# Kernel tuning notes

Measured on AMD Instinct MI355X. Metric: run time of the kernel, lower is better.

Reference implementation:

```python
import jax, jax.numpy as jnp
import numpy as np

HIDDEN = 4096
N_HEADS = 32
N_KV_HEADS = 8
HEAD_DIM = HIDDEN // N_HEADS  # 128
GROUPS = N_HEADS // N_KV_HEADS  # 4
SEQ = 2048


def setup_inputs() -> dict:
    key = jax.random.key(0)
    k1, k2, k3 = jax.random.split(key, 3)
    positions = jnp.arange(SEQ, dtype=jnp.int32)
    hidden_states = jax.random.normal(k1, (SEQ, HIDDEN), dtype=jnp.float32) * 0.02
    Wqkv = jax.random.normal(k2, (HIDDEN, (N_HEADS + 2 * N_KV_HEADS) * HEAD_DIM), dtype=jnp.float32) * 0.02
    Wo = jax.random.normal(k3, (N_HEADS * HEAD_DIM, HIDDEN), dtype=jnp.float32) * 0.02
    return {"positions": positions, "hidden_states": hidden_states, "Wqkv": Wqkv, "Wo": Wo}


def reference(positions, hidden_states, Wqkv, Wo):
    # forward unsqueezes to batch=1: x [1, S, D]
    x = hidden_states[None]
    S = x.shape[1]
    scale = HEAD_DIM ** -0.5

    qkv = jnp.einsum('bsd,de->bse', x, Wqkv)  # [1, S, (H + 2*KV)*Dh]
    q_sz = N_HEADS * HEAD_DIM
    kv_sz = N_KV_HEADS * HEAD_DIM
    q = qkv[..., :q_sz].reshape(1, S, N_KV_HEADS, GROUPS, HEAD_DIM)
    k = qkv[..., q_sz:q_sz + kv_sz].reshape(1, S, N_KV_HEADS, HEAD_DIM)
    v = qkv[..., q_sz + kv_sz:].reshape(1, S, N_KV_HEADS, HEAD_DIM)

    # grouped-query causal attention (ring attention on 1 device == flash causal GQA)
    scores = jnp.einsum('bqhgd,bkhd->bhgqk', q, k) * scale  # [1, KV, G, S, S]
    causal = jnp.tril(jnp.ones((S, S), dtype=bool))
    scores = jnp.where(causal, scores, jnp.finfo(scores.dtype).min)
    probs = jax.nn.softmax(scores, axis=-1)
    out = jnp.einsum('bhgqk,bkhd->bqhgd', probs, v)  # [1, S, KV, G, Dh]
    out = out.reshape(1, S, N_HEADS * HEAD_DIM)
    return jnp.einsum('bse,ed->bsd', out, Wo)  # [1, S, D]
```

## Files before the change

### kernel.cpp

```cpp
#include <hip/hip_runtime.h>


#define S_LEN 2048
#define DMODEL 4096
#define EQKV 6144
#define NHEADS 32
#define NKV 8
#define HDIM 128

using bf16x8 = __attribute__((ext_vector_type(8))) short;
using f32x4  = __attribute__((ext_vector_type(4))) float;

__device__ __forceinline__ ushort f2bf(float f) {
  unsigned u = __float_as_uint(f);
  u += 0x7fffu + ((u >> 16) & 1u);
  return (ushort)(u >> 16);
}

__device__ __forceinline__ void gll16(const void* g, void* l) {
  __builtin_amdgcn_global_load_lds(
      (const __attribute__((address_space(1))) unsigned int*)g,
      (__attribute__((address_space(3))) unsigned int*)l, 16, 0, 0);
}

__global__ __launch_bounds__(256) void cvt_f32_bf16(const float* __restrict__ in,
                                                    ushort* __restrict__ out, int n4) {
  int idx = blockIdx.x * 256 + threadIdx.x;
  if (idx < n4) {
    float4 v = ((const float4*)in)[idx];
    ushort4 o;
    o.x = f2bf(v.x); o.y = f2bf(v.y); o.z = f2bf(v.z); o.w = f2bf(v.w);
    ((ushort4*)out)[idx] = o;
  }
}

__global__ __launch_bounds__(256) void transpose_cvt(const float* __restrict__ W,
                                                     ushort* __restrict__ WT,
                                                     int K, int N) {
  __shared__ float t[32][33];
  const int kb = blockIdx.x * 32, nb = blockIdx.y * 32;
  const int tx = threadIdx.x & 31, ty = threadIdx.x >> 5;
#pragma unroll
  for (int i = 0; i < 4; ++i)
    t[ty + i * 8][tx] = W[(size_t)(kb + ty + i * 8) * N + nb + tx];
  __syncthreads();
#pragma unroll
  for (int i = 0; i < 4; ++i)
    WT[(size_t)(nb + ty + i * 8) * K + kb + tx] = f2bf(t[tx][ty + i * 8]);
}

__global__ __launch_bounds__(256) void vtrans(const ushort* __restrict__ QKV,
                                              ushort* __restrict__ VTg) {
  __shared__ ushort T[64][72];
  const int kv0 = blockIdx.x * 64;
  const int by = blockIdx.y;
  const int hk = by >> 1, dl0 = (by & 1) * 64;
#pragma unroll
  for (int t = 0; t < 4; ++t) {
    int C = t * 256 + threadIdx.x;
    int r = C >> 4, s = C & 15;
    *(ushort4*)&T[r][s * 4] =
        *(const ushort4*)(QKV + (size_t)(kv0 + r) * EQKV + 5120 + by * 64 + s * 4);
  }
  __syncthreads();
#pragma unroll
  for (int t = 0; t < 4; ++t) {
    int C = t * 256 + threadIdx.x;
    int d = C >> 4, kc = C & 15;
    ushort4 o;
    o.x = T[kc * 4 + 0][d]; o.y = T[kc * 4 + 1][d];
    o.z = T[kc * 4 + 2][d]; o.w = T[kc * 4 + 3][d];
    *(ushort4*)(VTg + (size_t)hk * 262144 + (size_t)(dl0 + d) * 2048 + kv0 + kc * 4) = o;
  }
}

template <bool OUT_BF16>
__global__ __launch_bounds__(256) void gemm_bt(const ushort* __restrict__ A,
                                               const ushort* __restrict__ BT,
                                               void* __restrict__ Cv,
                                               int M, int N, int K, int nbx) {
  __shared__ __align__(16) ushort At[4096];
  __shared__ __align__(16) ushort Bt[4096];
  const int tid = threadIdx.x;
  const int lane = tid & 63, w = tid >> 6;
  const int g = lane >> 4, i = lane & 15;
  const int wr = w >> 1, wc = w & 1;
  const int cpx = gridDim.x >> 3;
  const int sw = ((int)blockIdx.x & 7) * cpx + ((int)blockIdx.x >> 3);
  const int row0 = (sw % nbx) * 128, col0 = (sw / nbx) * 128;

  f32x4 acc[4][4] = {};

  for (int k0 = 0; k0 < K; k0 += 32) {
#pragma unroll
    for (int t = 0; t < 2; ++t) {
      int c = (w * 2 + t) * 64 + lane;
      int r = c >> 2, s = c & 3;
      gll16(A + (size_t)(row0 + r) * K + k0 + s * 8, At + (w * 2 + t) * 512);
      gll16(BT + (size_t)(col0 + r) * K + k0 + s * 8, Bt + (w * 2 + t) * 512);
    }
    __syncthreads();
    bf16x8 af[4], bfr[4];
#pragma unroll
    for (int mi = 0; mi < 4; ++mi)
      af[mi] = *(const bf16x8*)(At + (wr * 64 + mi * 16 + i) * 32 + g * 8);
#pragma unroll
    for (int ni = 0; ni < 4; ++ni)
      bfr[ni] = *(const bf16x8*)(Bt + (wc * 64 + ni * 16 + i) * 32 + g * 8);
#pragma unroll
    for (int mi = 0; mi < 4; ++mi)
#pragma unroll
      for (int ni = 0; ni < 4; ++ni)
        acc[mi][ni] = __builtin_amdgcn_mfma_f32_16x16x32_bf16(af[mi], bfr[ni],
                                                              acc[mi][ni], 0, 0, 0);
    __syncthreads();
  }
#pragma unroll
  for (int mi = 0; mi < 4; ++mi)
#pragma unroll
    for (int ni = 0; ni < 4; ++ni) {
      int r_ = row0 + wr * 64 + mi * 16 + g * 4;
      int c_ = col0 + wc * 64 + ni * 16 + i;
#pragma unroll
      for (int r = 0; r < 4; ++r) {
        if (OUT_BF16)
          ((ushort*)Cv)[(size_t)(r_ + r) * N + c_] = f2bf(acc[mi][ni][r]);
        else
          ((float*)Cv)[(size_t)(r_ + r) * N + c_] = acc[mi][ni][r];
      }
    }
}

__global__ __launch_bounds__(256) void attn_fwd(const ushort* __restrict__ QKV,
                                                const ushort* __restrict__ VTg,
                                                ushort* __restrict__ AO) {
  __shared__ __align__(16) char smem[32768];
  __shared__ ushort Pt[4][64 * 33];
  char* Ks = smem;
  char* Vs = smem + 16384;
  const int tid = threadIdx.x;
  const int lane = tid & 63, w = tid >> 6;
  const int g = lane >> 4, i = lane & 15;

  const int b = blockIdx.x;
  const int hk = b & 7;
  const int idx = b >> 3;
  const int h = hk * 4 + (idx & 3);
  const int qt = 15 - (idx >> 2);
  const int qb = qt * 128 + w * 32;
  const float scale = 0.08838834764831845f;
  const float NEGINF = -1.0e30f;

  const ushort* Kg = QKV + 4096 + hk * HDIM;
  const ushort* Vg = VTg + (size_t)hk * 262144;
  ushort* Pw = Pt[w];

  bf16x8 qf[2][4];
#pragma unroll
  for (int nt = 0; nt < 2; ++nt)
#pragma unroll
    for (int ks = 0; ks < 4; ++ks)
      qf[nt][ks] = *(const bf16x8*)(QKV + (size_t)(qb + nt * 16 + i) * EQKV +
                                    h * HDIM + ks * 32 + g * 8);

  f32x4 ot[8][2] = {};
  float m_i[2] = {-1.0e30f, -1.0e30f}, l_i[2] = {0.f, 0.f};

  const int nkb = (qt + 1) * 2;
  for (int kb = 0; kb < nkb; ++kb) {
    const int kv0 = kb * 64;
#pragma unroll
    for (int t = 0; t < 4; ++t) {
      int C = t * 256 + tid;
      int row = C >> 4, slot = C & 15;
      uint4 kv = *(const uint4*)(Kg + (size_t)(kv0 + row) * EQKV + slot * 8);
      *(uint4*)(Ks + row * 256 + ((slot * 16) ^ ((row & 7) << 4))) = kv;
      int d = C >> 3, sl = C & 7;
      uint4 vv = *(const uint4*)(Vg + (size_t)d * 2048 + kv0 + sl * 8);
      *(uint4*)(Vs + d * 128 + ((sl * 16) ^ ((d & 7) << 4))) = vv;
    }
    __syncthreads();
    if (kv0 <= qb + 31) {
      f32x4 st[4][2] = {};
#pragma unroll
      for (int ks = 0; ks < 4; ++ks)
#pragma unroll
        for (int mt = 0; mt < 4; ++mt) {
          int row = mt * 16 + i;
          bf16x8 kf = *(const bf16x8*)(Ks + row * 256 +
                                       ((ks * 64 + g * 16) ^ ((row & 7) << 4)));
#pragma unroll
          for (int nt = 0; nt < 2; ++nt)
            st[mt][nt] = __builtin_amdgcn_mfma_f32_16x16x32_bf16(kf, qf[nt][ks],
                                                                 st[mt][nt], 0, 0, 0);
        }
      float al[2];
#pragma unroll
      for (int nt = 0; nt < 2; ++nt) {
        const int qg = qb + nt * 16 + i;
        float ps[4][4];
        float tm = NEGINF;
#pragma unroll
        for (int mt = 0; mt < 4; ++mt)
#pragma unroll
          for (int r = 0; r < 4; ++r) {
            int kvg = kv0 + mt * 16 + g * 4 + r;
            float s = st[mt][nt][r] * scale;
            s = (kvg > qg) ? NEGINF : s;
            ps[mt][r] = s;
            tm = fmaxf(tm, s);
          }
        tm = fmaxf(tm, __shfl_xor(tm, 16));
        tm = fmaxf(tm, __shfl_xor(tm, 32));
        float mn = fmaxf(m_i[nt], tm);
        float a = __expf(m_i[nt] - mn);
        float rs = 0.f;
#pragma unroll
        for (int mt = 0; mt < 4; ++mt)
#pragma unroll
          for (int r = 0; r < 4; ++r) {
            ps[mt][r] = __expf(ps[mt][r] - mn);
            rs += ps[mt][r];
          }
        rs += __shfl_xor(rs, 16);
        rs += __shfl_xor(rs, 32);
        l_i[nt] = l_i[nt] * a + rs;
        m_i[nt] = mn;
        al[nt] = a;
#pragma unroll
        for (int mt = 0; mt < 4; ++mt)
#pragma unroll
          for (int r = 0; r < 4; ++r)
            Pw[(mt * 16 + g * 4 + r) * 33 + nt * 16 + i] = f2bf(ps[mt][r]);
      }
#pragma unroll
      for (int md = 0; md < 8; ++md)
#pragma unroll
        for (int nt = 0; nt < 2; ++nt)
#pragma unroll
          for (int r = 0; r < 4; ++r)
            ot[md][nt][r] *= al[nt];
      bf16x8 ptf[2][2];
#pragma unroll
      for (int kst = 0; kst < 2; ++kst)
#pragma unroll
        for (int nt = 0; nt < 2; ++nt) {
          union { ushort e[8]; bf16x8 v; } uu;
#pragma unroll
          for (int j = 0; j < 8; ++j)
            uu.e[j] = Pw[(kst * 32 + g * 8 + j) * 33 + nt * 16 + i];
          ptf[kst][nt] = uu.v;
        }
#pragma unroll
      for (int md = 0; md < 8; ++md)
#pragma unroll
        for (int kst = 0; kst < 2; ++kst) {
          int row = md * 16 + i;
          bf16x8 vf = *(const bf16x8*)(Vs + row * 128 +
                                       ((kst * 64 + g * 16) ^ ((row & 7) << 4)));
#pragma unroll
          for (int nt = 0; nt < 2; ++nt)
            ot[md][nt] = __builtin_amdgcn_mfma_f32_16x16x32_bf16(vf, ptf[kst][nt],
                                                                 ot[md][nt], 0, 0, 0);
        }
    }
    __syncthreads();
  }
  char* Sw = smem + w * 8192;
#pragma unroll
  for (int md = 0; md < 8; ++md)
#pragma unroll
    for (int nt = 0; nt < 2; ++nt)
#pragma unroll
      for (int r = 0; r < 4; ++r) {
        int row = nt * 16 + i, col = md * 16 + g * 4 + r;
        *(ushort*)(Sw + row * 256 + ((col * 2) ^ ((row & 7) << 4))) =
            f2bf(ot[md][nt][r] / l_i[nt]);
      }
#pragma unroll
  for (int t = 0; t < 8; ++t) {
    int c = t * 64 + lane;
    int row = c >> 4, sl = c & 15;
    uint4 v = *(const uint4*)(Sw + row * 256 + ((sl * 16) ^ ((row & 7) << 4)));
    *(uint4*)(AO + (size_t)(qb + row) * DMODEL + h * HDIM + sl * 8) = v;
  }
}

extern "C" void kernel_launch(void* const* d_in, const int* in_sizes, int n_in,
                              void* d_out, int out_size, void* d_ws, size_t ws_size,
                              hipStream_t stream) {
  const float* hidden = (const float*)d_in[1];
  const float* Wqkv   = (const float*)d_in[2];
  const float* Wo     = (const float*)d_in[3];
  float* out = (float*)d_out;

  char* ws = (char*)d_ws;
  const size_t off_Xb    = 0;
  const size_t off_QKV   = 16777216;
  const size_t off_AO    = 41943040;
  const size_t off_WqkvT = 58720256;
  const size_t off_WoT   = 109051904;
  ushort* Xb    = (ushort*)(ws + off_Xb);
  ushort* VTg   = (ushort*)(ws + off_Xb);
  ushort* QKVb  = (ushort*)(ws + off_QKV);
  ushort* AO    = (ushort*)(ws + off_AO);
  ushort* WqkvT = (ushort*)(ws + off_WqkvT);
  ushort* WoT   = (ushort*)(ws + off_WoT);

  cvt_f32_bf16<<<(S_LEN * DMODEL / 4 + 255) / 256, 256, 0, stream>>>(
      hidden, Xb, S_LEN * DMODEL / 4);
  transpose_cvt<<<dim3(DMODEL / 32, EQKV / 32), 256, 0, stream>>>(Wqkv, WqkvT,
                                                                  DMODEL, EQKV);
  transpose_cvt<<<dim3(DMODEL / 32, DMODEL / 32), 256, 0, stream>>>(Wo, WoT,
                                                                    DMODEL, DMODEL);
  gemm_bt<true><<<768, 256, 0, stream>>>(Xb, WqkvT, (void*)QKVb,
                                         S_LEN, EQKV, DMODEL, 16);
  vtrans<<<dim3(32, 16), 256, 0, stream>>>(QKVb, VTg);
  attn_fwd<<<512, 256, 0, stream>>>(QKVb, VTg, AO);
  gemm_bt<false><<<512, 256, 0, stream>>>(AO, WoT, (void*)out,
                                          S_LEN, DMODEL, DMODEL, 16);
}
```

Before: 581.1 us.

## Widen GEMM K-tile with XOR-swizzled LDS and transpose attention P scratch for vector access

The GEMM now stages a 64-wide K slice per iteration instead of 32, with an XOR swizzle on the LDS column chunks. This halves the number of barriers per K and is meant to cut LDS bank conflicts. In attention, the P scratch buffer is stored transposed with a padded stride of 72. P is then written with 8-byte vector stores and read back as 16-byte vector loads, replacing scalar ushort stores and eight scalar loads per fragment. The trade-off is doubled GEMM LDS use, which may lower occupancy, and a risk of new bank conflicts from the 72 stride.

Result: faster. 521.1 us (-10.3%).

```diff
diff --git a/kernel.cpp b/kernel.cpp
--- a/kernel.cpp
+++ b/kernel.cpp
@@ -79,8 +79,8 @@
                                                const ushort* __restrict__ BT,
                                                void* __restrict__ Cv,
                                                int M, int N, int K, int nbx) {
-  __shared__ __align__(16) ushort At[4096];
-  __shared__ __align__(16) ushort Bt[4096];
+  __shared__ __align__(16) ushort At[128 * 64];
+  __shared__ __align__(16) ushort Bt[128 * 64];
   const int tid = threadIdx.x;
   const int lane = tid & 63, w = tid >> 6;
   const int g = lane >> 4, i = lane & 15;
@@ -91,28 +91,36 @@
 
   f32x4 acc[4][4] = {};
 
-  for (int k0 = 0; k0 < K; k0 += 32) {
-#pragma unroll
-    for (int t = 0; t < 2; ++t) {
-      int c = (w * 2 + t) * 64 + lane;
-      int r = c >> 2, s = c & 3;
-      gll16(A + (size_t)(row0 + r) * K + k0 + s * 8, At + (w * 2 + t) * 512);
-      gll16(BT + (size_t)(col0 + r) * K + k0 + s * 8, Bt + (w * 2 + t) * 512);
+  for (int k0 = 0; k0 < K; k0 += 64) {
+#pragma unroll
+    for (int t = 0; t < 4; ++t) {
+      int c = (w * 4 + t) * 64 + lane;
+      int r = c >> 3, s = c & 7;
+      int ss = s ^ (r & 7);
+      gll16(A + (size_t)(row0 + r) * K + k0 + ss * 8, At + (w * 4 + t) * 512);
+      gll16(BT + (size_t)(col0 + r) * K + k0 + ss * 8, Bt + (w * 4 + t) * 512);
     }
     __syncthreads();
-    bf16x8 af[4], bfr[4];
-#pragma unroll
-    for (int mi = 0; mi < 4; ++mi)
-      af[mi] = *(const bf16x8*)(At + (wr * 64 + mi * 16 + i) * 32 + g * 8);
-#pragma unroll
-    for (int ni = 0; ni < 4; ++ni)
-      bfr[ni] = *(const bf16x8*)(Bt + (wc * 64 + ni * 16 + i) * 32 + g * 8);
-#pragma unroll
-    for (int mi = 0; mi < 4; ++mi)
-#pragma unroll
-      for (int ni = 0; ni < 4; ++ni)
-        acc[mi][ni] = __builtin_amdgcn_mfma_f32_16x16x32_bf16(af[mi], bfr[ni],
-                                                              acc[mi][ni], 0, 0, 0);
+#pragma unroll
+    for (int kk = 0; kk < 2; ++kk) {
+      bf16x8 af[4], bfr[4];
+#pragma unroll
+      for (int mi = 0; mi < 4; ++mi) {
+        int row = wr * 64 + mi * 16 + i;
+        af[mi] = *(const bf16x8*)(At + row * 64 + (((kk * 4 + g) ^ (row & 7)) * 8));
+      }
+#pragma unroll
+      for (int ni = 0; ni < 4; ++ni) {
+        int row = wc * 64 + ni * 16 + i;
+        bfr[ni] = *(const bf16x8*)(Bt + row * 64 + (((kk * 4 + g) ^ (row & 7)) * 8));
+      }
+#pragma unroll
+      for (int mi = 0; mi < 4; ++mi)
+#pragma unroll
+        for (int ni = 0; ni < 4; ++ni)
+          acc[mi][ni] = __builtin_amdgcn_mfma_f32_16x16x32_bf16(af[mi], bfr[ni],
+                                                                acc[mi][ni], 0, 0, 0);
+    }
     __syncthreads();
   }
 #pragma unroll
@@ -135,7 +143,7 @@
                                                 const ushort* __restrict__ VTg,
                                                 ushort* __restrict__ AO) {
   __shared__ __align__(16) char smem[32768];
-  __shared__ ushort Pt[4][64 * 33];
+  __shared__ __align__(16) ushort Pt[4][32 * 72];
   char* Ks = smem;
   char* Vs = smem + 16384;
   const int tid = threadIdx.x;
@@ -228,10 +236,12 @@
         m_i[nt] = mn;
         al[nt] = a;
 #pragma unroll
-        for (int mt = 0; mt < 4; ++mt)
-#pragma unroll
-          for (int r = 0; r < 4; ++r)
-            Pw[(mt * 16 + g * 4 + r) * 33 + nt * 16 + i] = f2bf(ps[mt][r]);
+        for (int mt = 0; mt < 4; ++mt) {
+          ushort4 p4;
+          p4.x = f2bf(ps[mt][0]); p4.y = f2bf(ps[mt][1]);
+          p4.z = f2bf(ps[mt][2]); p4.w = f2bf(ps[mt][3]);
+          *(ushort4*)&Pw[(nt * 16 + i) * 72 + mt * 16 + g * 4] = p4;
+        }
       }
 #pragma unroll
       for (int md = 0; md < 8; ++md)
@@ -244,13 +254,8 @@
 #pragma unroll
       for (int kst = 0; kst < 2; ++kst)
 #pragma unroll
-        for (int nt = 0; nt < 2; ++nt) {
-          union { ushort e[8]; bf16x8 v; } uu;
-#pragma unroll
-          for (int j = 0; j < 8; ++j)
-            uu.e[j] = Pw[(kst * 32 + g * 8 + j) * 33 + nt * 16 + i];
-          ptf[kst][nt] = uu.v;
-        }
+        for (int nt = 0; nt < 2; ++nt)
+          ptf[kst][nt] = *(const bf16x8*)&Pw[(nt * 16 + i) * 72 + kst * 32 + g * 8];
 #pragma unroll
       for (int md = 0; md < 8; ++md)
 #pragma unroll
```
